# Optimization experiments

Measured on AMD Instinct MI355X. Metric: run time of the kernel, lower is better.

Reference implementation:

```python
import jax, jax.numpy as jnp
import numpy as np

D_MODEL, D_STATE, D_CONV, EXPAND = 1024, 16, 4, 2
D_INNER = EXPAND * D_MODEL
BATCH, SEQ = 2, 2048


def setup_inputs() -> dict:
    key = jax.random.key(0)
    ks = jax.random.split(key, 10)
    s = lambda fan_in: 1.0 / np.sqrt(fan_in)
    return {
        "x": jax.random.normal(ks[0], (BATCH, SEQ, D_MODEL), jnp.float32),
        "W_in": jax.random.normal(ks[1], (2 * D_INNER, D_MODEL), jnp.float32) * s(D_MODEL),
        "w_conv": jax.random.normal(ks[2], (D_INNER, D_CONV), jnp.float32) * s(D_CONV),
        "b_conv": jax.random.normal(ks[3], (D_INNER,), jnp.float32) * 0.02,
        "W_x": jax.random.normal(ks[4], (D_INNER + 2 * D_STATE, D_INNER), jnp.float32) * s(D_INNER),
        "W_dt": jax.random.normal(ks[5], (D_INNER, D_INNER), jnp.float32) * s(D_INNER),
        "b_dt": jax.random.normal(ks[6], (D_INNER,), jnp.float32) * 0.02,
        "A_log": jnp.log(jax.random.uniform(ks[7], (D_INNER, D_STATE), jnp.float32, 1e-4, 1.0)),
        "D": jnp.ones((D_INNER,), jnp.float32),
        "W_out": jax.random.normal(ks[8], (D_MODEL, D_INNER), jnp.float32) * s(D_INNER),
    }


def _depthwise_causal_conv(x, w, b):
    # x: (B, L, C), w: (C, K), causal (left-pad K-1), matches conv1d(padding=K-1)[..., :L]
    K = w.shape[1]
    L = x.shape[1]
    xp = jnp.pad(x, ((0, 0), (K - 1, 0), (0, 0)))
    out = b
    for k in range(K):  # K is tiny (4)
        out = out + xp[:, k:k + L, :] * w[:, k]
    return out


def _selective_scan(x, delta, Bm, Cm, A, Dv):
    # x, delta: (B, L, d_inner); Bm, Cm: (B, L, d_state)
    def step(state, inp):
        x_t, d_t, B_t, C_t = inp  # (B,d_inner),(B,d_inner),(B,d_state),(B,d_state)
        decay = jnp.exp(d_t[..., None] * A)          # (B, d_inner, d_state)
        state = decay * state + B_t[:, None, :] * x_t[..., None]
        y_t = jnp.einsum('bds,bs->bd', state, C_t) + x_t * Dv
        return state, y_t

    init = jnp.zeros((x.shape[0], x.shape[2], A.shape[1]), x.dtype)
    xs = tuple(jnp.swapaxes(a, 0, 1) for a in (x, delta, Bm, Cm))
    _, ys = jax.lax.scan(step, init, xs)             # ys: (L, B, d_inner)
    return jnp.swapaxes(ys, 0, 1)


def reference(x, W_in, w_conv, b_conv, W_x, W_dt, b_dt, A_log, D, W_out):
    silu = jax.nn.silu
    xz = x @ W_in.T                                   # (B, L, 2*d_inner)
    x_inner, z = jnp.split(xz, 2, axis=-1)
    x_conv = silu(_depthwise_causal_conv(x_inner, w_conv, b_conv))
    x_dbl = x_conv @ W_x.T                            # (B, L, d_inner + 2*d_state)
    delta, Bm, Cm = jnp.split(x_dbl, [D_INNER, D_INNER + D_STATE], axis=-1)
    delta = jax.nn.softplus(delta @ W_dt.T + b_dt)
    A = -jnp.exp(A_log.astype(jnp.float32))
    y = _selective_scan(x_conv, delta, Bm, Cm, A, D)
    y = y * silu(z)
    return y @ W_out.T
```

## Files before the change

kernel.cpp:

```cpp
#include <hip/hip_runtime.h>
#include <hip/hip_bf16.h>


#define BATCH 2
#define SEQ   2048
#define DM    1024
#define DI    2048
#define DS    16
#define T_TOK (BATCH * SEQ)

#define CL 64
#define NC 32

typedef __bf16 v8bf __attribute__((ext_vector_type(8)));
typedef float  v4f  __attribute__((ext_vector_type(4)));

__device__ __forceinline__ void gld16(const void* g, void* l) {
    __builtin_amdgcn_global_load_lds(
        (const __attribute__((address_space(1))) void*)g,
        (__attribute__((address_space(3))) void*)l, 16, 0, 0);
}

__device__ __forceinline__ float b2f(__hip_bfloat16 v) { return __bfloat162float(v); }

__device__ __forceinline__ int is_bf(const void* Dref) {
    return ((const unsigned*)Dref)[0] == 0x3F803F80u;
}

__device__ __forceinline__ float load_in(const void* p, size_t i, int isbf) {
    return isbf ? b2f(((const __hip_bfloat16*)p)[i]) : ((const float*)p)[i];
}

__device__ __forceinline__ float softplus_f(float x) {
    return (x > 15.f) ? x : __logf(1.f + __expf(x));
}

#define NBIG0 (T_TOK * DM)
#define NBIG1 (4096 * DM)
#define NBIG2 (DI * DI)
#define NBIG3 (DM * DI)
#define NB_BIG 7168
#define NB_TR  1024
#define NB_SM  184
#define NB_PAD 128
#define NB_ALL (NB_BIG + NB_TR + NB_SM + NB_PAD)

#define LOG2E 1.44269504088896340736f

__global__ __launch_bounds__(256) void convert_all(
    const void* __restrict__ s0, const void* __restrict__ s1,
    const void* __restrict__ s2, const void* __restrict__ s3,
    __hip_bfloat16* __restrict__ d0, __hip_bfloat16* __restrict__ d1,
    __hip_bfloat16* __restrict__ d2, __hip_bfloat16* __restrict__ d3,
    const void* __restrict__ wconv, const void* __restrict__ bconv,
    const void* __restrict__ bdt, const void* __restrict__ dv,
    const void* __restrict__ A_log,
    __hip_bfloat16* __restrict__ wconvb, __hip_bfloat16* __restrict__ bconvb,
    __hip_bfloat16* __restrict__ bdtb, __hip_bfloat16* __restrict__ db,
    float* __restrict__ Amat,
    const void* __restrict__ Wx, __hip_bfloat16* __restrict__ WxdT,
    __hip_bfloat16* __restrict__ Wxp)
{
    __shared__ __bf16 t[64][72];
    const int isbf = is_bf(dv);
    const int bid = blockIdx.x;

    if (bid < NB_BIG) {
        if (isbf) return;
        size_t e = ((size_t)bid * 256 + threadIdx.x) * 8;
        const float* src; __hip_bfloat16* dst;
        if (e < NBIG0)                      { src = (const float*)s0 + e;                 dst = d0 + e; }
        else if (e < NBIG0 + NBIG1)         { e -= NBIG0; src = (const float*)s1 + e;     dst = d1 + e; }
        else if (e < NBIG0 + NBIG1 + NBIG2) { e -= NBIG0 + NBIG1; src = (const float*)s2 + e; dst = d2 + e; }
        else                                { e -= NBIG0 + NBIG1 + NBIG2; src = (const float*)s3 + e; dst = d3 + e; }
        const float4 a = *(const float4*)src;
        const float4 b = *(const float4*)(src + 4);
        __bf16 o[8] = {(__bf16)a.x,(__bf16)a.y,(__bf16)a.z,(__bf16)a.w,
                       (__bf16)b.x,(__bf16)b.y,(__bf16)b.z,(__bf16)b.w};
        *(uint4*)dst = *(uint4*)&o[0];
    } else if (bid < NB_BIG + NB_TR) {
        const int b2 = bid - NB_BIG;
        const int bi = (b2 >> 5) * 64;
        const int bj = (b2 & 31) * 64;
        const int rr = threadIdx.x >> 3;
        const int c0 = (threadIdx.x & 7) * 8;
#pragma unroll
        for (int k = 0; k < 2; k++) {
            const int r = rr + k * 32;
            const size_t src = (size_t)(bi + r) * DI + bj + c0;
            __bf16 o[8];
            if (isbf) {
                *(uint4*)&o[0] = *(const uint4*)((const __hip_bfloat16*)Wx + src);
            } else {
                const float* s = (const float*)Wx + src;
                const float4 a = *(const float4*)s;
                const float4 b = *(const float4*)(s + 4);
                o[0]=(__bf16)a.x; o[1]=(__bf16)a.y; o[2]=(__bf16)a.z; o[3]=(__bf16)a.w;
                o[4]=(__bf16)b.x; o[5]=(__bf16)b.y; o[6]=(__bf16)b.z; o[7]=(__bf16)b.w;
            }
            *(uint4*)&t[r][c0] = *(uint4*)&o[0];
        }
        __syncthreads();
#pragma unroll
        for (int k = 0; k < 2; k++) {
            const int dr = rr + k * 32;
            __bf16 o[8];
#pragma unroll
            for (int j = 0; j < 8; j++) o[j] = t[c0 + j][dr];
            *(uint4*)(WxdT + (size_t)(bj + dr) * DI + bi + c0) = *(uint4*)&o[0];
        }
    } else if (bid < NB_BIG + NB_TR + NB_SM) {
        const int i = (bid - (NB_BIG + NB_TR)) * 256 + threadIdx.x;
        if (i < 8192)        wconvb[i]        = __float2bfloat16(load_in(wconv, i, isbf));
        else if (i < 10240)  bconvb[i - 8192] = __float2bfloat16(load_in(bconv, i - 8192, isbf));
        else if (i < 12288)  bdtb[i - 10240]  = __float2bfloat16(load_in(bdt, i - 10240, isbf));
        else if (i < 14336)  db[i - 12288]    = __float2bfloat16(load_in(dv, i - 12288, isbf));
        else if (i < 47104)  Amat[i - 14336]  = -__expf(load_in(A_log, i - 14336, isbf)) * LOG2E;
    } else {
        const size_t e = ((size_t)(bid - (NB_BIG + NB_TR + NB_SM)) * 256 + threadIdx.x) * 8;
        if (e >= (size_t)128 * DI) return;
        const size_t base = (size_t)2048 * DI;
        if (e >= (size_t)32 * DI) {
            __bf16 z[8] = {};
            *(uint4*)(Wxp + base + e) = *(uint4*)&z[0];
            return;
        }
        if (isbf) {
            *(uint4*)(Wxp + base + e) = *(const uint4*)((const __hip_bfloat16*)Wx + base + e);
        } else {
            const float* src = (const float*)Wx + base + e;
            const float4 a = *(const float4*)src;
            const float4 b = *(const float4*)(src + 4);
            __bf16 o[8] = {(__bf16)a.x,(__bf16)a.y,(__bf16)a.z,(__bf16)a.w,
                           (__bf16)b.x,(__bf16)b.y,(__bf16)b.z,(__bf16)b.w};
            *(uint4*)(Wxp + base + e) = *(uint4*)&o[0];
        }
    }
}

template <int MODE, int TN>
__device__ __forceinline__ void gemm_core(
    const __hip_bfloat16* __restrict__ A, const __hip_bfloat16* __restrict__ Bw,
    void* __restrict__ out0, void* __restrict__ out1,
    int isbf, int id, int nx, int nblk, int N, int K)
{
    constexpr int NF = TN / 32;
    constexpr int ASLOT = 512;
    constexpr int BSLOT = TN * 4;
    __shared__ v8bf Asv[2 * ASLOT];
    __shared__ v8bf Bsv[2 * BSLOT];

    const int ny = nblk / nx;
    int bxs, bys;
    if (((nx & 3) == 0) && ((ny & 1) == 0)) {
        const int rx = nx >> 2, ry = ny >> 1;
        const int xcd = id & 7, lid = id >> 3;
        bxs = (xcd & 3) * rx + lid % rx;
        bys = (xcd >> 2) * ry + lid / rx;
    } else {
        const int sid = (id & 7) * (nblk >> 3) + (id >> 3);
        bxs = sid % nx;
        bys = sid / nx;
    }

    const int tid  = threadIdx.x;
    const int bm   = bys * 128;
    const int bn   = bxs * TN;
    const int w    = tid >> 6;
    const int lane = tid & 63;
    const int wm   = (w >> 1) * 64;
    const int wn   = (w & 1) * (TN / 2);
    const int lrow  = lane & 15;
    const int lquad = lane >> 4;

    v4f acc[4][NF];
#pragma unroll
    for (int i = 0; i < 4; i++)
#pragma unroll
        for (int j = 0; j < NF; j++) acc[i][j] = (v4f){0.f, 0.f, 0.f, 0.f};

    const int r0 = tid >> 2;
    const int q0 = (tid & 3) ^ ((r0 >> 1) & 3);
    const __hip_bfloat16* gA0 = A  + (size_t)(bm + r0) * K + q0 * 8;
    const __hip_bfloat16* gA1 = A  + (size_t)(bm + 64 + r0) * K + q0 * 8;
    const __hip_bfloat16* gB0 = Bw + (size_t)(bn + r0) * K + q0 * 8;
    const __hip_bfloat16* gB1 = Bw + (size_t)(bn + 64 + r0) * K + q0 * 8;
    char* lA0 = (char*)Asv + tid * 16;
    char* lA1 = (char*)Asv + 4096 + tid * 16;
    char* lB0 = (char*)Bsv + tid * 16;
    char* lB1 = (char*)Bsv + 4096 + tid * 16;

    const int swz = lquad ^ ((lrow >> 1) & 3);
    int sA[4], sB[NF];
#pragma unroll
    for (int i = 0; i < 4; i++) sA[i] = (wm + i * 16 + lrow) * 4 + swz;
#pragma unroll
    for (int i = 0; i < NF; i++) sB[i] = (wn + i * 16 + lrow) * 4 + swz;

    const int NIT = K >> 5;
    gld16(gA0, lA0);
    gld16(gA1, lA1);
    gld16(gB0, lB0);
    if (TN == 128) gld16(gB1, lB1);

    int k = 32;
    for (int it = 0; it < NIT; ++it) {
        const int cb = it & 1;
        __syncthreads();
        if (it + 1 < NIT) {
            const int pa = (cb ^ 1) * 8192;
            const int pb = (cb ^ 1) * (BSLOT * 16);
            gld16(gA0 + k, lA0 + pa);
            gld16(gA1 + k, lA1 + pa);
            gld16(gB0 + k, lB0 + pb);
            if (TN == 128) gld16(gB1 + k, lB1 + pb);
            k += 32;
        }
        const int ca = cb * ASLOT;
        const int cbb = cb * BSLOT;
        v8bf af[4], bfr[NF];
#pragma unroll
        for (int i = 0; i < 4; i++)
            af[i] = Asv[ca + sA[i]];
#pragma unroll
        for (int i = 0; i < NF; i++)
            bfr[i] = Bsv[cbb + sB[i]];
#pragma unroll
        for (int mi = 0; mi < 4; mi++)
#pragma unroll
            for (int ni = 0; ni < NF; ni++)
                acc[mi][ni] = __builtin_amdgcn_mfma_f32_16x16x32_bf16(
                    af[mi], bfr[ni], acc[mi][ni], 0, 0, 0);
    }

#pragma unroll
    for (int mi = 0; mi < 4; mi++) {
#pragma unroll
        for (int ni = 0; ni < NF; ni++) {
#pragma unroll
            for (int r = 0; r < 4; r++) {
                const int grow = bm + wm + mi * 16 + lquad * 4 + r;
                const int gcol = bn + wn + ni * 16 + lrow;
                const float v = acc[mi][ni][r];
                if (MODE == 0) {
                    ((__hip_bfloat16*)out0)[(size_t)grow * N + gcol] = __float2bfloat16(v);
                } else if (MODE == 1) {
                    if (gcol < 2048) {
                        ((__hip_bfloat16*)out0)[(size_t)grow * 2048 + gcol] = __float2bfloat16(v);
                    } else if (gcol < 2080) {
                        ((float*)out1)[(size_t)grow * 32 + (gcol - 2048)] = v;
                    }
                } else {
                    if (isbf)
                        ((__hip_bfloat16*)out0)[(size_t)grow * N + gcol] = __float2bfloat16(v);
                    else
                        ((float*)out0)[(size_t)grow * N + gcol] = v;
                }
            }
        }
    }
}

template <int MODE, int TN>
__global__ __launch_bounds__(256) void gemm_single(
    const __hip_bfloat16* __restrict__ Ac, const void* __restrict__ Araw,
    const __hip_bfloat16* __restrict__ Bc, const void* __restrict__ Braw,
    void* __restrict__ out0, void* __restrict__ out1,
    const void* __restrict__ Dref, int N, int K)
{
    const int isbf = is_bf(Dref);
    const __hip_bfloat16* A = (isbf && Araw) ? (const __hip_bfloat16*)Araw : Ac;
    const __hip_bfloat16* B = (isbf && Braw) ? (const __hip_bfloat16*)Braw : Bc;
    const int nx = gridDim.x;
    const int nblk = gridDim.x * gridDim.y;
    const int id = blockIdx.y * nx + blockIdx.x;
    gemm_core<MODE, TN>(A, B, out0, out1, isbf, id, nx, nblk, N, K);
}

__global__ __launch_bounds__(256) void gemm_dual(
    const __hip_bfloat16* __restrict__ A1c, const void* __restrict__ A1raw,
    const __hip_bfloat16* __restrict__ B1c, const void* __restrict__ B1raw,
    void* __restrict__ o1,
    const __hip_bfloat16* __restrict__ A2c, const void* __restrict__ A2raw,
    const __hip_bfloat16* __restrict__ B2,
    void* __restrict__ o2,
    const void* __restrict__ Dref)
{
    const int isbf = is_bf(Dref);
    const __hip_bfloat16* A;
    const __hip_bfloat16* B;
    void* o;
    int id, nx, nblk, N, K;
    if (blockIdx.x < 1024) {
        A = (isbf && A1raw) ? (const __hip_bfloat16*)A1raw : A1c;
        B = (isbf && B1raw) ? (const __hip_bfloat16*)B1raw : B1c;
        o = o1; id = blockIdx.x; nx = 32; nblk = 1024; N = 4096; K = 1024;
    } else {
        A = (isbf && A2raw) ? (const __hip_bfloat16*)A2raw : A2c;
        B = B2;
        o = o2; id = blockIdx.x - 1024; nx = 16; nblk = 256; N = 2048; K = 2048;
    }
    gemm_core<0, 128>(A, B, o, nullptr, isbf, id, nx, nblk, N, K);
}

__global__ __launch_bounds__(256) void conv_silu(
    const __hip_bfloat16* __restrict__ xz,
    const __hip_bfloat16* __restrict__ wconv,
    const __hip_bfloat16* __restrict__ bconv,
    __hip_bfloat16* __restrict__ xconv)
{
    const int idx = blockIdx.x * 256 + threadIdx.x;
    const int c8  = (idx & 255) << 3;
    const int g   = idx >> 8;
    const int tg0 = g << 2;
    const int tl0 = tg0 & (SEQ - 1);

    __bf16 wl[32], bl[8];
    *(uint4*)&wl[0]  = *(const uint4*)(wconv + c8 * 4);
    *(uint4*)&wl[8]  = *(const uint4*)(wconv + c8 * 4 + 8);
    *(uint4*)&wl[16] = *(const uint4*)(wconv + c8 * 4 + 16);
    *(uint4*)&wl[24] = *(const uint4*)(wconv + c8 * 4 + 24);
    *(uint4*)&bl[0]  = *(const uint4*)(bconv + c8);

    __bf16 rows[7][8];
#pragma unroll
    for (int j = 0; j < 7; j++) {
        const int ts = tl0 - 3 + j;
        if (ts >= 0) {
            *(uint4*)&rows[j][0] = *(const uint4*)(xz + (size_t)(tg0 - 3 + j) * 4096 + c8);
        } else {
            __bf16 z[8] = {};
            *(uint4*)&rows[j][0] = *(uint4*)&z[0];
        }
    }

#pragma unroll
    for (int i = 0; i < 4; i++) {
        float acc[8];
#pragma unroll
        for (int cc = 0; cc < 8; cc++) acc[cc] = (float)bl[cc];
#pragma unroll
        for (int k = 0; k < 4; k++)
#pragma unroll
            for (int cc = 0; cc < 8; cc++)
                acc[cc] += (float)wl[cc * 4 + k] * (float)rows[i + k][cc];
        __bf16 o[8];
#pragma unroll
        for (int cc = 0; cc < 8; cc++) {
            const float s = acc[cc] / (1.f + __expf(-acc[cc]));
            o[cc] = (__bf16)s;
        }
        *(uint4*)(xconv + (size_t)(tg0 + i) * DI + c8) = *(uint4*)&o[0];
    }
}

__global__ __launch_bounds__(256) void scan_p1(
    const __hip_bfloat16* __restrict__ dlin, const __hip_bfloat16* __restrict__ xconv,
    const float* __restrict__ BCg, const float* __restrict__ Amat,
    const __hip_bfloat16* __restrict__ bdt,
    float* __restrict__ Pws, float* __restrict__ Sws)
{
    const int d = blockIdx.x * 256 + threadIdx.x;
    const int c = blockIdx.y;
    const int b = blockIdx.z;
    const int tg0 = b * SEQ + c * CL;

    __shared__ float bc[CL * 32];
    for (int i = threadIdx.x; i < CL * 32; i += 256) bc[i] = BCg[(size_t)tg0 * 32 + i];
    __syncthreads();

    float Areg[DS];
#pragma unroll
    for (int s = 0; s < DS; s++) Areg[s] = Amat[d * DS + s];
    const float bd = b2f(bdt[d]);

    float dlsum = 0.f;
    float S[DS];
#pragma unroll
    for (int s = 0; s < DS; s++) S[s] = 0.f;

    for (int i = 0; i < CL; i++) {
        const size_t tg = tg0 + i;
        const float dl = softplus_f(b2f(dlin[tg * DI + d]) + bd);
        const float x  = b2f(xconv[tg * DI + d]);
        dlsum += dl;
#pragma unroll
        for (int s = 0; s < DS; s++) {
            const float e = exp2f(dl * Areg[s]);
            S[s] = e * S[s] + bc[i * 32 + s] * x;
        }
    }

    const size_t base = (((size_t)b * NC + c) * DI + d) * DS;
#pragma unroll
    for (int s = 0; s < DS; s += 4) {
        *(float4*)(Pws + base + s) = make_float4(
            exp2f(dlsum * Areg[s]),     exp2f(dlsum * Areg[s + 1]),
            exp2f(dlsum * Areg[s + 2]), exp2f(dlsum * Areg[s + 3]));
        *(float4*)(Sws + base + s) = make_float4(S[s], S[s+1], S[s+2], S[s+3]);
    }
}

__global__ void scan_p2(float* __restrict__ Pws, float* __restrict__ Sws) {
    const int idx = blockIdx.x * 256 + threadIdx.x;
    const int b  = idx >> 15;
    const int ds = idx & 32767;
    float carry = 0.f;
    for (int c = 0; c < NC; c++) {
        const size_t a = (((size_t)b * NC + c) << 15) + ds;
        const float p  = Pws[a];
        const float sv = Sws[a];
        Sws[a] = carry;
        carry = p * carry + sv;
    }
}

__global__ __launch_bounds__(256) void scan_p3(
    const __hip_bfloat16* __restrict__ dlin, const __hip_bfloat16* __restrict__ xconv,
    const float* __restrict__ BCg, const float* __restrict__ Amat,
    const __hip_bfloat16* __restrict__ bdt,
    const float* __restrict__ Sws, const __hip_bfloat16* __restrict__ xz,
    const __hip_bfloat16* __restrict__ Dv, __hip_bfloat16* __restrict__ yg)
{
    const int d = blockIdx.x * 256 + threadIdx.x;
    const int c = blockIdx.y;
    const int b = blockIdx.z;
    const int tg0 = b * SEQ + c * CL;

    __shared__ float bc[CL * 32];
    for (int i = threadIdx.x; i < CL * 32; i += 256) bc[i] = BCg[(size_t)tg0 * 32 + i];
    __syncthreads();

    float Areg[DS];
#pragma unroll
    for (int s = 0; s < DS; s++) Areg[s] = Amat[d * DS + s];
    const float bd = b2f(bdt[d]);

    const size_t base = (((size_t)b * NC + c) * DI + d) * DS;
    float S[DS];
#pragma unroll
    for (int s = 0; s < DS; s += 4) {
        const float4 v = *(const float4*)(Sws + base + s);
        S[s] = v.x; S[s+1] = v.y; S[s+2] = v.z; S[s+3] = v.w;
    }
    const float Dd = b2f(Dv[d]);

    for (int i = 0; i < CL; i++) {
        const size_t tg = tg0 + i;
        const float dl = softplus_f(b2f(dlin[tg * DI + d]) + bd);
        const float x  = b2f(xconv[tg * DI + d]);
        float y = 0.f;
#pragma unroll
        for (int s = 0; s < DS; s++) {
            const float e = exp2f(dl * Areg[s]);
            S[s] = e * S[s] + bc[i * 32 + s] * x;
            y += S[s] * bc[i * 32 + 16 + s];
        }
        y += x * Dd;
        const float z = b2f(xz[tg * 4096 + 2048 + d]);
        const float g = z / (1.f + __expf(-z));
        yg[tg * DI + d] = __float2bfloat16(y * g);
    }
}

extern "C" void kernel_launch(void* const* d_in, const int* in_sizes, int n_in,
                              void* d_out, int out_size, void* d_ws, size_t ws_size,
                              hipStream_t stream)
{
    const void* x_raw     = d_in[0];
    const void* W_in_raw  = d_in[1];
    const void* wconv_raw = d_in[2];
    const void* bconv_raw = d_in[3];
    const void* W_x_raw   = d_in[4];
    const void* W_dt_raw  = d_in[5];
    const void* b_dt_raw  = d_in[6];
    const void* A_log_raw = d_in[7];
    const void* D_raw     = d_in[8];
    const void* W_out_raw = d_in[9];

    char* ws = (char*)d_ws;
    size_t off = 0;
    auto alloc = [&](size_t bytes) { char* p = ws + off; off += (bytes + 255) & ~(size_t)255; return p; };
    __hip_bfloat16* XB    = (__hip_bfloat16*)alloc((size_t)T_TOK * DM * 2);
    __hip_bfloat16* WINB  = (__hip_bfloat16*)alloc((size_t)4096 * DM * 2);
    __hip_bfloat16* WDTB  = (__hip_bfloat16*)alloc((size_t)DI * DI * 2);
    __hip_bfloat16* WOUTB = (__hip_bfloat16*)alloc((size_t)DM * DI * 2);
    __hip_bfloat16* WCONVB= (__hip_bfloat16*)alloc((size_t)DI * 4 * 2);
    __hip_bfloat16* BCONVB= (__hip_bfloat16*)alloc((size_t)DI * 2);
    __hip_bfloat16* BDTB  = (__hip_bfloat16*)alloc((size_t)DI * 2);
    __hip_bfloat16* DB    = (__hip_bfloat16*)alloc((size_t)DI * 2);
    __hip_bfloat16* XZ    = (__hip_bfloat16*)alloc((size_t)T_TOK * 4096 * 2);
    __hip_bfloat16* XCONV = (__hip_bfloat16*)alloc((size_t)T_TOK * DI * 2);
    __hip_bfloat16* WXDT  = (__hip_bfloat16*)alloc((size_t)DI * DI * 2);
    __hip_bfloat16* WXPAD = (__hip_bfloat16*)alloc((size_t)2176 * DI * 2);
    float*          BC    = (float*)alloc((size_t)T_TOK * 32 * 4);
    __hip_bfloat16* DELTA = (__hip_bfloat16*)alloc((size_t)T_TOK * DI * 2);
    float*          AMAT  = (float*)alloc((size_t)DI * DS * 4);
    float*          PWS   = (float*)alloc((size_t)BATCH * NC * DI * DS * 4);
    float*          SWS   = (float*)alloc((size_t)BATCH * NC * DI * DS * 4);
    __hip_bfloat16* YG    = (__hip_bfloat16*)alloc((size_t)T_TOK * DI * 2);

    convert_all<<<NB_ALL, 256, 0, stream>>>(
        x_raw, W_in_raw, W_dt_raw, W_out_raw, XB, WINB, WDTB, WOUTB,
        wconv_raw, bconv_raw, b_dt_raw, D_raw, A_log_raw,
        WCONVB, BCONVB, BDTB, DB, AMAT,
        W_x_raw, WXDT, WXPAD);

    gemm_dual<<<1280, 256, 0, stream>>>(
        XB, x_raw, WINB, W_in_raw, XZ,
        WDTB, W_dt_raw, WXDT, WXPAD, D_raw);

    conv_silu<<<T_TOK / 4, 256, 0, stream>>>(XZ, WCONVB, BCONVB, XCONV);

    gemm_single<1, 128><<<dim3(17, 32), 256, 0, stream>>>(
        XCONV, nullptr, WXPAD, nullptr, DELTA, BC, D_raw, 2176, 2048);

    scan_p1<<<dim3(DI / 256, NC, BATCH), 256, 0, stream>>>(
        DELTA, XCONV, BC, AMAT, BDTB, PWS, SWS);
    scan_p2<<<(BATCH * DI * DS) / 256, 256, 0, stream>>>(PWS, SWS);
    scan_p3<<<dim3(DI / 256, NC, BATCH), 256, 0, stream>>>(
        DELTA, XCONV, BC, AMAT, BDTB, SWS, XZ, DB, YG);

    gemm_single<3, 64><<<dim3(16, 32), 256, 0, stream>>>(
        YG, nullptr, WOUTB, W_out_raw, d_out, nullptr, D_raw, 1024, 2048);
}
```

Baseline: 455.2 us.

## Add 256x256 8-wave pipelined GEMM for input projection, split dual GEMM

Adds a new 512-thread GEMM kernel with 256x256 output tiles, a 4-stage LDS ring fed by direct global-to-LDS loads, swizzled LDS addressing, interleaved MFMA phases and setprio scheduling. It replaces the input projection (x @ W_in^T) half of the fused dual GEMM. The W_dt weight precompute moves into its own gemm_single launch. The larger tile is meant to improve operand reuse and hide load latency on the biggest GEMM. In exchange it uses one extra launch, drops the co-scheduling of the two GEMMs, and launches only 256 blocks, which may leave CUs underused.

```diff
diff --git a/kernel.cpp b/kernel.cpp
--- a/kernel.cpp
+++ b/kernel.cpp
@@ -138,6 +138,143 @@
     }
 }
 
+template <int KDIM>
+__global__ __launch_bounds__(512, 2) void gemm8p(
+    const __hip_bfloat16* __restrict__ Ac, const void* __restrict__ Araw,
+    const __hip_bfloat16* __restrict__ Bc, const void* __restrict__ Braw,
+    void* __restrict__ out0,
+    const void* __restrict__ Dref,
+    int N)
+{
+    constexpr int NT = KDIM >> 5;
+    __shared__ v8bf lds[8192];
+
+    const int isbf = is_bf(Dref);
+    const __hip_bfloat16* A  = (isbf && Araw) ? (const __hip_bfloat16*)Araw : Ac;
+    const __hip_bfloat16* Bw = (isbf && Braw) ? (const __hip_bfloat16*)Braw : Bc;
+
+    const int nx = gridDim.x;
+    const int nblk = nx * gridDim.y;
+    const int id = blockIdx.y * nx + blockIdx.x;
+    const int sid = (id & 7) * (nblk >> 3) + (id >> 3);
+    const int bm = (sid / nx) * 256;
+    const int bn = (sid % nx) * 256;
+
+    const int tid   = threadIdx.x;
+    const int lane  = tid & 63;
+    const int w     = tid >> 6;
+    const int wr    = (w >> 2) * 128;
+    const int wc    = (w & 3) * 64;
+    const int lrow  = lane & 15;
+    const int lquad = lane >> 4;
+    const int swz   = lquad ^ ((lrow >> 1) & 3);
+
+    v4f acc[8][4];
+#pragma unroll
+    for (int i = 0; i < 8; i++)
+#pragma unroll
+        for (int j = 0; j < 4; j++) acc[i][j] = (v4f){0.f, 0.f, 0.f, 0.f};
+
+    const int r0 = tid >> 2;
+    const int q0 = (tid & 3) ^ ((r0 >> 1) & 3);
+    const __hip_bfloat16* gA0 = A  + (size_t)(bm + r0) * KDIM + q0 * 8;
+    const __hip_bfloat16* gA1 = gA0 + (size_t)128 * KDIM;
+    const __hip_bfloat16* gB0 = Bw + (size_t)(bn + r0) * KDIM + q0 * 8;
+    const __hip_bfloat16* gB1 = gB0 + (size_t)128 * KDIM;
+    char* lbase = (char*)&lds[0] + tid * 16;
+
+    int sA[8], sB[4];
+#pragma unroll
+    for (int i = 0; i < 8; i++) sA[i] = (wr + i * 16 + lrow) * 4 + swz;
+#pragma unroll
+    for (int i = 0; i < 4; i++) sB[i] = 1024 + (wc + i * 16 + lrow) * 4 + swz;
+
+#define STAGE8(kt, b) do {                         \
+        const size_t ko_ = (size_t)(kt) * 32;      \
+        char* d_ = lbase + (b) * 32768;            \
+        gld16(gA0 + ko_, d_);                      \
+        gld16(gA1 + ko_, d_ + 8192);               \
+        gld16(gB0 + ko_, d_ + 16384);              \
+        gld16(gB1 + ko_, d_ + 24576);              \
+    } while (0)
+
+    STAGE8(0, 0);
+    STAGE8(1, 1);
+    STAGE8(2, 2);
+    asm volatile("s_waitcnt vmcnt(8)" ::: "memory");
+    __builtin_amdgcn_s_barrier();
+
+#pragma unroll 4
+    for (int t = 0; t < NT; ++t) {
+        const int cb = t & 3;
+        const v8bf* buf = &lds[0] + cb * 2048;
+        const int pf = t + 3;
+        char* pdst = lbase + (pf & 3) * 32768;
+        const size_t pko = (size_t)pf * 32;
+
+        v8bf af0[4], af1[4], bfr[4];
+#pragma unroll
+        for (int i = 0; i < 4; i++) af0[i] = buf[sA[i]];
+#pragma unroll
+        for (int i = 0; i < 4; i++) bfr[i] = buf[sB[i]];
+        if (pf < NT) {
+            gld16(gA0 + pko, pdst);
+            gld16(gA1 + pko, pdst + 8192);
+        }
+        __builtin_amdgcn_s_barrier();
+        asm volatile("s_waitcnt lgkmcnt(0)" ::: "memory");
+        __builtin_amdgcn_sched_barrier(0);
+        __builtin_amdgcn_s_setprio(1);
+#pragma unroll
+        for (int mi = 0; mi < 4; mi++)
+#pragma unroll
+            for (int ni = 0; ni < 4; ni++)
+                acc[mi][ni] = __builtin_amdgcn_mfma_f32_16x16x32_bf16(
+                    af0[mi], bfr[ni], acc[mi][ni], 0, 0, 0);
+        __builtin_amdgcn_s_setprio(0);
+        __builtin_amdgcn_s_barrier();
+
+#pragma unroll
+        for (int i = 0; i < 4; i++) af1[i] = buf[sA[4 + i]];
+        if (pf < NT) {
+            gld16(gB0 + pko, pdst + 16384);
+            gld16(gB1 + pko, pdst + 24576);
+            asm volatile("s_waitcnt vmcnt(8)" ::: "memory");
+        } else if (t + 3 == NT) {
+            asm volatile("s_waitcnt vmcnt(4)" ::: "memory");
+        } else if (t + 2 == NT) {
+            asm volatile("s_waitcnt vmcnt(0)" ::: "memory");
+        }
+        __builtin_amdgcn_s_barrier();
+        asm volatile("s_waitcnt lgkmcnt(0)" ::: "memory");
+        __builtin_amdgcn_sched_barrier(0);
+        __builtin_amdgcn_s_setprio(1);
+#pragma unroll
+        for (int mi = 0; mi < 4; mi++)
+#pragma unroll
+            for (int ni = 0; ni < 4; ni++)
+                acc[4 + mi][ni] = __builtin_amdgcn_mfma_f32_16x16x32_bf16(
+                    af1[mi], bfr[ni], acc[4 + mi][ni], 0, 0, 0);
+        __builtin_amdgcn_s_setprio(0);
+        __builtin_amdgcn_s_barrier();
+    }
+#undef STAGE8
+
+#pragma unroll
+    for (int mi = 0; mi < 8; mi++) {
+#pragma unroll
+        for (int ni = 0; ni < 4; ni++) {
+#pragma unroll
+            for (int r = 0; r < 4; r++) {
+                const int grow = bm + wr + mi * 16 + lquad * 4 + r;
+                const int gcol = bn + wc + ni * 16 + lrow;
+                ((__hip_bfloat16*)out0)[(size_t)grow * N + gcol] =
+                    __float2bfloat16(acc[mi][ni][r]);
+            }
+        }
+    }
+}
+
 template <int MODE, int TN>
 __device__ __forceinline__ void gemm_core(
     const __hip_bfloat16* __restrict__ A, const __hip_bfloat16* __restrict__ Bw,
@@ -275,32 +412,6 @@
     const int nblk = gridDim.x * gridDim.y;
     const int id = blockIdx.y * nx + blockIdx.x;
     gemm_core<MODE, TN>(A, B, out0, out1, isbf, id, nx, nblk, N, K);
-}
-
-__global__ __launch_bounds__(256) void gemm_dual(
-    const __hip_bfloat16* __restrict__ A1c, const void* __restrict__ A1raw,
-    const __hip_bfloat16* __restrict__ B1c, const void* __restrict__ B1raw,
-    void* __restrict__ o1,
-    const __hip_bfloat16* __restrict__ A2c, const void* __restrict__ A2raw,
-    const __hip_bfloat16* __restrict__ B2,
-    void* __restrict__ o2,
-    const void* __restrict__ Dref)
-{
-    const int isbf = is_bf(Dref);
-    const __hip_bfloat16* A;
-    const __hip_bfloat16* B;
-    void* o;
-    int id, nx, nblk, N, K;
-    if (blockIdx.x < 1024) {
-        A = (isbf && A1raw) ? (const __hip_bfloat16*)A1raw : A1c;
-        B = (isbf && B1raw) ? (const __hip_bfloat16*)B1raw : B1c;
-        o = o1; id = blockIdx.x; nx = 32; nblk = 1024; N = 4096; K = 1024;
-    } else {
-        A = (isbf && A2raw) ? (const __hip_bfloat16*)A2raw : A2c;
-        B = B2;
-        o = o2; id = blockIdx.x - 1024; nx = 16; nblk = 256; N = 2048; K = 2048;
-    }
-    gemm_core<0, 128>(A, B, o, nullptr, isbf, id, nx, nblk, N, K);
 }
 
 __global__ __launch_bounds__(256) void conv_silu(
@@ -506,9 +617,11 @@
         WCONVB, BCONVB, BDTB, DB, AMAT,
         W_x_raw, WXDT, WXPAD);
 
-    gemm_dual<<<1280, 256, 0, stream>>>(
-        XB, x_raw, WINB, W_in_raw, XZ,
-        WDTB, W_dt_raw, WXDT, WXPAD, D_raw);
+    gemm8p<1024><<<dim3(16, 16), 512, 0, stream>>>(
+        XB, x_raw, WINB, W_in_raw, XZ, D_raw, 4096);
+
+    gemm_single<0, 128><<<dim3(16, 16), 256, 0, stream>>>(
+        WDTB, W_dt_raw, WXDT, nullptr, WXPAD, nullptr, D_raw, 2048, 2048);
 
     conv_silu<<<T_TOK / 4, 256, 0, stream>>>(XZ, WCONVB, BCONVB, XCONV);
 
```

Measured after the change: 442.6 us. -2.8%, faster.
